# Performance work log

Measured on AMD Instinct MI355X. Metric: run time of the kernel, lower is better.

Reference implementation:

```python
import jax, jax.numpy as jnp
import numpy as np

B, T, FD, NH, NC, NOUT = 32, 512, 256, 1024, 512, 8


def setup_inputs() -> dict:
    key = jax.random.key(0)
    ks = jax.random.split(key, 12)
    s = lambda k, sh, sc=0.05: (jax.random.normal(k, sh, jnp.float32) * sc)
    return dict(
        x=jax.random.normal(ks[0], (B, T, FD), jnp.float32),
        lens=jax.random.randint(ks[1], (B,), T // 2, T + 1, jnp.int32),
        W1=s(ks[2], (NH, FD)), b1=jnp.zeros((NH,), jnp.float32),
        g1=jnp.ones((NH,), jnp.float32), be1=jnp.zeros((NH,), jnp.float32),
        W2=s(ks[3], (NH, NH)), b2=jnp.zeros((NH,), jnp.float32),
        g2=jnp.ones((NH,), jnp.float32), be2=jnp.zeros((NH,), jnp.float32),
        lstm_wih=s(ks[4], (2, 2, 4 * NC, NH)),   # [layer, dir, 4H, in]
        lstm_whh=s(ks[5], (2, 2, 4 * NC, NC)),   # [layer, dir, 4H, H]
        lstm_bih=s(ks[6], (2, 2, 4 * NC)),
        lstm_bhh=s(ks[7], (2, 2, 4 * NC)),
        w_u=s(ks[8], (2 * NC,)), b_u=jnp.zeros((), jnp.float32),
        Wc=s(ks[9], (NOUT, 2 * NC)), bc=jnp.zeros((NOUT,), jnp.float32),
    )


def _layernorm(x, g, b, eps=1e-5):
    m = x.mean(-1, keepdims=True)
    v = ((x - m) ** 2).mean(-1, keepdims=True)
    return (x - m) / jnp.sqrt(v + eps) * g + b


def _lrelu(z):
    return jnp.where(z >= 0, z, 0.01 * z)  # LeakyReLU default slope


def _lstm_dir(x, wih, whh, bih, bhh):
    # x: [B,T,in] -> h: [B,T,H]; torch gate order i,f,g,o
    Bz = x.shape[0]
    H = whh.shape[1]
    xp = jnp.einsum('bti,gi->btg', x, wih) + bih + bhh  # [B,T,4H]

    def step(carry, xt):
        h, c = carry
        gates = xt + h @ whh.T
        i, f, g, o = jnp.split(gates, 4, axis=-1)
        c = jax.nn.sigmoid(f) * c + jax.nn.sigmoid(i) * jnp.tanh(g)
        h = jax.nn.sigmoid(o) * jnp.tanh(c)
        return (h, c), h

    h0 = jnp.zeros((Bz, H), x.dtype)
    _, hs = jax.lax.scan(step, (h0, h0), xp.transpose(1, 0, 2))
    return hs.transpose(1, 0, 2)


def _bilstm(x, wih, whh, bih, bhh):
    # params indexed [dir, ...]; backward dir processes the full padded
    # sequence reversed (original feeds unpacked pad_sequence to nn.LSTM)
    hf = _lstm_dir(x, wih[0], whh[0], bih[0], bhh[0])
    hb = _lstm_dir(x[:, ::-1], wih[1], whh[1], bih[1], bhh[1])[:, ::-1]
    return jnp.concatenate([hf, hb], axis=-1)


def reference(x, lens, W1, b1, g1, be1, W2, b2, g2, be2,
              lstm_wih, lstm_whh, lstm_bih, lstm_bhh, w_u, b_u, Wc, bc):
    Tn = x.shape[1]
    # extract MLP (dropout = identity in eval)
    h = _lrelu(_layernorm(x @ W1.T + b1, g1, be1))
    h = _lrelu(_layernorm(h @ W2.T + b2, g2, be2))
    # pad_sequence zero-pads AFTER extract -> zero out pad positions
    mask = jnp.arange(Tn)[None, :] < lens[:, None]  # [B,T]
    h = h * mask[..., None]
    # 2-layer bidirectional LSTM over the full padded sequence
    h = _bilstm(h, lstm_wih[0], lstm_whh[0], lstm_bih[0], lstm_bhh[0])
    h = _bilstm(h, lstm_wih[1], lstm_whh[1], lstm_bih[1], lstm_bhh[1])
    # Attn with window_len=1: per-step linear score, masked softmax, weighted sum
    scores = h @ w_u + b_u                          # [B,T]
    scores = jnp.where(mask, scores, -jnp.inf)
    alpha = jax.nn.softmax(scores, axis=-1)
    pooled = jnp.einsum('bt,btd->bd', alpha, h)     # [B, 2*NC]
    return pooled @ Wc.T + bc
```

## Files before the change

kernel.cpp:

```cpp
#include <hip/hip_runtime.h>
#include <stdint.h>
#include <stddef.h>


typedef short  short8  __attribute__((ext_vector_type(8)));
typedef short  short4v __attribute__((ext_vector_type(4)));
typedef float  float4v __attribute__((ext_vector_type(4)));
typedef unsigned long long u64;

__device__ inline float b2f(short x){
  union { unsigned u; float f; } v; v.u = ((unsigned)(unsigned short)x) << 16; return v.f;
}
__device__ inline short f2b(float f){
  union { float f; unsigned u; } v; v.f = f;
  unsigned r = (v.u + 0x7fffu + ((v.u >> 16) & 1u)) >> 16;
  return (short)r;
}
__device__ inline float sigm(float x){ return 1.f / (1.f + __expf(-x)); }
__device__ inline float tanh_(float x){ return 2.f / (1.f + __expf(-2.f*x)) - 1.f; }

typedef const __attribute__((address_space(1))) unsigned gu32;
typedef __attribute__((address_space(3))) unsigned lu32;
__device__ inline void gld16(const void* g, void* l){
  __builtin_amdgcn_global_load_lds((gu32*)g, (lu32*)l, 16, 0, 0);
}

__global__ __launch_bounds__(256) void detect_f32(
    const unsigned short* __restrict__ p, unsigned* __restrict__ flag)
{
  const int tid = threadIdx.x;
  unsigned h = 0;
  for (int i = tid; i < 1024; i += 256){
    const unsigned e = (p[i] >> 7) & 0xFFu;
    if (e >= 0xC0u) ++h;
  }
#pragma unroll
  for (int off=32; off>0; off>>=1) h += __shfl_xor(h, off, 64);
  __shared__ unsigned sh[4];
  if ((tid&63)==0) sh[tid>>6] = h;
  __syncthreads();
  if (tid==0) *flag = (sh[0]+sh[1]+sh[2]+sh[3] >= 8u) ? 1u : 0u;
}

struct CvtArgs {
  const void* src[16];
  short*      dst[16];
  int         n[16];
  int         boff[17];
};

__global__ __launch_bounds__(256) void to_bf16_batch(
    CvtArgs a, const unsigned* __restrict__ flag)
{
  const int b = blockIdx.x;
  int lo = 0, hi = 15;
  while (lo < hi){
    const int mid = (lo + hi + 1) >> 1;
    if (b >= a.boff[mid]) lo = mid; else hi = mid - 1;
  }
  const int i   = lo;
  const int idx = (b - a.boff[i])*256 + (int)threadIdx.x;
  if (idx >= a.n[i]) return;
  if (*flag) a.dst[i][idx] = f2b(((const float*)a.src[i])[idx]);
  else       a.dst[i][idx] = ((const short*)a.src[i])[idx];
}

__global__ __launch_bounds__(256) void gemm_bt(
    const short* __restrict__ A, const short* __restrict__ W,
    short* __restrict__ C, const short* __restrict__ bias1,
    const short* __restrict__ bias2, int N, int K)
{
  __shared__ __align__(16) short lA[128*32];
  __shared__ __align__(16) short lW[128*32];
  __shared__ __align__(16) short eps[2*16*136];
  const int tid  = threadIdx.x;
  const int lane = tid & 63, wv = tid >> 6;
  const int wm = wv >> 1, wn = wv & 1;
  const int quad = lane >> 4, l15 = lane & 15;
  const long m0 = (long)blockIdx.y * 128, n0 = (long)blockIdx.x * 128;

  float4v acc[4][4];
#pragma unroll
  for (int i=0;i<4;++i)
#pragma unroll
    for (int j=0;j<4;++j) acc[i][j] = (float4v)0.f;

  const int srow = wv*16 + (lane >> 2);
  const int scol = ((lane & 3) ^ (srow & 3)) * 8;
  char* lAb = (char*)&lA[0] + wv*1024;
  char* lWb = (char*)&lW[0] + wv*1024;
  const int rchunk = (quad ^ (l15 & 3)) * 8;

  const int nkt = K >> 5;
  for (int kt = 0; kt < nkt; ++kt) {
    __syncthreads();
    {
      const short* gA0 = A + (m0 + srow) * (long)K + kt*32 + scol;
      const short* gW0 = W + (n0 + srow) * (long)K + kt*32 + scol;
      gld16(gA0,                lAb);
      gld16(gA0 + 64*(long)K,   lAb + 4096);
      gld16(gW0,                lWb);
      gld16(gW0 + 64*(long)K,   lWb + 4096);
    }
    __syncthreads();
    short8 af[4], bfr[4];
#pragma unroll
    for (int i=0;i<4;++i) af[i]  = *(const short8*)&lA[(wm*64 + i*16 + l15)*32 + rchunk];
#pragma unroll
    for (int j=0;j<4;++j) bfr[j] = *(const short8*)&lW[(wn*64 + j*16 + l15)*32 + rchunk];
#pragma unroll
    for (int i=0;i<4;++i)
#pragma unroll
      for (int j=0;j<4;++j)
        acc[i][j] = __builtin_amdgcn_mfma_f32_16x16x32_bf16(af[i], bfr[j], acc[i][j], 0, 0, 0);
  }

  float bs[4];
#pragma unroll
  for (int j=0;j<4;++j){
    const long n = n0 + wn*64 + j*16 + l15;
    bs[j] = b2f(bias1[n]);
    if (bias2) bs[j] += b2f(bias2[n]);
  }
  const int eh = tid >> 7, er = (tid >> 3) & 15, ec = tid & 7;
  short* erd = &eps[(eh*16 + er)*136 + ec*16];
  short* ewr = &eps[wm*16*136 + wn*64 + l15];
#pragma unroll
  for (int i=0;i<4;++i){
    if (i) __syncthreads();
#pragma unroll
    for (int j=0;j<4;++j)
#pragma unroll
      for (int g=0; g<4; ++g)
        ewr[(quad*4+g)*136 + j*16] = f2b(acc[i][j][g] + bs[j]);
    __syncthreads();
    short8 v0 = *(const short8*)erd;
    short8 v1 = *(const short8*)(erd + 8);
    short* cp = &C[(m0 + eh*64 + i*16 + er)*(long)N + n0 + ec*16];
    *(short8*)cp       = v0;
    *(short8*)(cp + 8) = v1;
  }
}

__global__ __launch_bounds__(256) void ln_lrelu(
    const short* __restrict__ X, const short* __restrict__ g,
    const short* __restrict__ be, short* __restrict__ out,
    const int* __restrict__ lens, const int domask)
{
  const int row = blockIdx.x, tid = threadIdx.x;
  const short* xr = X + (size_t)row * 1024;
  short4v xv = *(const short4v*)(xr + tid*4);
  float v[4];
#pragma unroll
  for (int k=0;k<4;++k) v[k] = b2f(xv[k]);
  float s  = v[0]+v[1]+v[2]+v[3];
  float sq = v[0]*v[0]+v[1]*v[1]+v[2]*v[2]+v[3]*v[3];
#pragma unroll
  for (int off=32; off>0; off>>=1){
    s  += __shfl_xor(s,  off, 64);
    sq += __shfl_xor(sq, off, 64);
  }
  __shared__ float red[8];
  if ((tid&63)==0){ red[tid>>6] = s; red[4+(tid>>6)] = sq; }
  __syncthreads();
  s  = red[0]+red[1]+red[2]+red[3];
  sq = red[4]+red[5]+red[6]+red[7];
  const float mean = s * (1.f/1024.f);
  const float var  = sq * (1.f/1024.f) - mean*mean;
  const float rstd = rsqrtf(var + 1e-5f);
  float zmul = 1.f;
  if (domask){ const int b = row >> 9, t = row & 511; if (t >= lens[b]) zmul = 0.f; }
  short4v o;
#pragma unroll
  for (int k=0;k<4;++k){
    const int n = tid*4 + k;
    float y = (v[k]-mean)*rstd*b2f(g[n]) + b2f(be[n]);
    y = (y >= 0.f) ? y : 0.01f*y;
    o[k] = f2b(y * zmul);
  }
  *(short4v*)(out + (size_t)row*1024 + tid*4) = o;
}

__global__ __launch_bounds__(256) void lstm_scan(
    const short* __restrict__ xp, const int xp_cols, const int dir0,
    const short* __restrict__ whh,
    u64* __restrict__ hstate,
    short* __restrict__ hout,
    const unsigned epoch)
{
  const int wg = blockIdx.x;
  const int dloc = wg >> 5, d = dir0 + dloc;
  const int u0 = (wg & 31) * 16;
  const int tid = threadIdx.x, lane = tid & 63, wv = tid >> 6;
  const int quad = lane >> 4, l15 = lane & 15;

  short8 af[16];
  {
    const short* wr = whh + ((size_t)d*2048 + wv*512 + u0 + l15)*512 + quad*8;
#pragma unroll
    for (int ks=0; ks<16; ++ks) af[ks] = *(const short8*)(wr + ks*32);
  }

  const int bb = tid >> 3, pp = tid & 7;
  float cstA = 0.f, cstB = 0.f;
  __shared__ __align__(16) unsigned hsh[2][32*260];
  __shared__ float gl[4][16][33];
  const unsigned tbase = epoch << 10;

  for (int step=0; step<512; ++step){
    const int t = d ? (511-step) : step;
    short4v x0, x1;
    {
      const size_t gb = (size_t)dloc*2048 + (size_t)wv*512 + u0 + quad*4;
      x0 = *(const short4v*)(xp + ((size_t)l15*512      + t)*xp_cols + gb);
      x1 = *(const short4v*)(xp + ((size_t)(l15+16)*512 + t)*xp_cols + gb);
    }
    unsigned* stg = &hsh[step&1][tid];
    if (step == 0){
#pragma unroll
      for (int k=0;k<32;++k) stg[k*260] = 0u;
    } else {
      const u64* hq = hstate + ((size_t)(d*2 + (step&1))<<13) + tid;
      const unsigned tgt = tbase + (unsigned)step;
      u64 v[32];
      for(;;){
        unsigned ok = 1u;
#pragma unroll
        for (int k=0;k<32;++k)
          v[k] = __hip_atomic_load(hq + (size_t)k*256,
                                   __ATOMIC_RELAXED, __HIP_MEMORY_SCOPE_AGENT);
#pragma unroll
        for (int k=0;k<32;++k) ok &= (unsigned)((unsigned)(v[k] >> 32) == tgt);
        if (ok) break;
        __builtin_amdgcn_s_sleep(1);
      }
#pragma unroll
      for (int k=0;k<32;++k) stg[k*260] = (unsigned)v[k];
    }
    __syncthreads();

    float4v acc0, acc1;
#pragma unroll
    for (int g=0; g<4; ++g){ acc0[g] = b2f(x0[g]); acc1[g] = b2f(x1[g]); }
    const short* hs = (const short*)&hsh[step&1][0];
#pragma unroll
    for (int ks=0; ks<16; ++ks){
      short8 b0 = *(const short8*)(hs + (size_t)l15*520      + ks*32 + quad*8);
      short8 b1 = *(const short8*)(hs + (size_t)(l15+16)*520 + ks*32 + quad*8);
      acc0 = __builtin_amdgcn_mfma_f32_16x16x32_bf16(af[ks], b0, acc0, 0, 0, 0);
      acc1 = __builtin_amdgcn_mfma_f32_16x16x32_bf16(af[ks], b1, acc1, 0, 0, 0);
    }
#pragma unroll
    for (int g=0; g<4; ++g){
      gl[wv][quad*4+g][l15]    = acc0[g];
      gl[wv][quad*4+g][l15+16] = acc1[g];
    }
    __syncthreads();

    float hv[2];
#pragma unroll
    for (int i=0; i<2; ++i){
      const int uu = 2*pp + i;
      const float gi = gl[0][uu][bb], gf = gl[1][uu][bb];
      const float gg = gl[2][uu][bb], go = gl[3][uu][bb];
      float& cref = i ? cstB : cstA;
      const float c = sigm(gf)*cref + sigm(gi)*tanh_(gg);
      cref = c;
      hv[i] = sigm(go) * tanh_(c);
    }
    const unsigned hw = (unsigned)(unsigned short)f2b(hv[0])
                      | ((unsigned)(unsigned short)f2b(hv[1]) << 16);
    const u64 pkt = ((u64)(tbase + (unsigned)step + 1u) << 32) | (u64)hw;
    __hip_atomic_store(hstate + ((size_t)(d*2 + ((step+1)&1))<<13)
                         + (size_t)bb*256 + (u0>>1) + pp,
                       pkt, __ATOMIC_RELAXED, __HIP_MEMORY_SCOPE_AGENT);
    *(unsigned*)&hout[((size_t)bb*512 + t)*1024 + d*512 + u0 + 2*pp] = hw;
  }
}

__global__ __launch_bounds__(256) void attn_cls(
    const short* __restrict__ hseq, const short* __restrict__ wu,
    const short* __restrict__ Wc, const short* __restrict__ bc,
    const int* __restrict__ lens, float* __restrict__ out)
{
  const int b = blockIdx.x, tid = threadIdx.x, lane = tid & 63, wv = tid >> 6;
  const int len = lens[b];
  __shared__ float wus[1024];
  __shared__ float sc[512];
  __shared__ float redx[8];
  __shared__ float pooled[1024];
  for (int i=tid; i<1024; i+=256) wus[i] = b2f(wu[i]);
  __syncthreads();
  const short* hb = hseq + (size_t)b*512*1024;
  for (int t=wv; t<512; t+=4){
    const short* hr = hb + (size_t)t*1024;
    float s = 0.f;
#pragma unroll
    for (int j=0;j<16;++j) s += b2f(hr[lane + j*64]) * wus[lane + j*64];
#pragma unroll
    for (int off=32; off>0; off>>=1) s += __shfl_xor(s, off, 64);
    if (lane==0) sc[t] = (t < len) ? s : -3.0e38f;
  }
  __syncthreads();
  float m = -3.0e38f;
  for (int i=tid;i<512;i+=256) m = fmaxf(m, sc[i]);
#pragma unroll
  for (int off=32; off>0; off>>=1) m = fmaxf(m, __shfl_xor(m, off, 64));
  if (lane==0) redx[wv] = m;
  __syncthreads();
  m = fmaxf(fmaxf(redx[0],redx[1]), fmaxf(redx[2],redx[3]));
  float ssum = 0.f;
  for (int i=tid;i<512;i+=256){
    float e = (i<len) ? __expf(sc[i]-m) : 0.f;
    sc[i] = e;
    ssum += e;
  }
#pragma unroll
  for (int off=32; off>0; off>>=1) ssum += __shfl_xor(ssum, off, 64);
  if (lane==0) redx[4+wv] = ssum;
  __syncthreads();
  ssum = redx[4]+redx[5]+redx[6]+redx[7];
  const float inv = 1.f/ssum;
  float4v pa = (float4v)0.f;
  const int k0 = tid*4;
  for (int t=0; t<len; ++t){
    const float a = sc[t];
    short4v hv = *(const short4v*)(hb + (size_t)t*1024 + k0);
    pa[0] += a*b2f(hv[0]); pa[1] += a*b2f(hv[1]);
    pa[2] += a*b2f(hv[2]); pa[3] += a*b2f(hv[3]);
  }
  pooled[k0+0] = pa[0]*inv; pooled[k0+1] = pa[1]*inv;
  pooled[k0+2] = pa[2]*inv; pooled[k0+3] = pa[3]*inv;
  __syncthreads();
  const int j = tid >> 5, l32 = tid & 31;
  float s2 = 0.f;
  for (int kk=l32; kk<1024; kk+=32) s2 += b2f(Wc[j*1024+kk]) * pooled[kk];
#pragma unroll
  for (int off=16; off>0; off>>=1) s2 += __shfl_xor(s2, off, 32);
  if (l32==0) out[b*8+j] = s2 + b2f(bc[j]);
}

extern "C" void kernel_launch(void* const* d_in, const int* in_sizes, int n_in,
                              void* d_out, int out_size, void* d_ws, size_t ws_size,
                              hipStream_t stream)
{
  (void)in_sizes; (void)n_in; (void)out_size;
  const int*   lens = (const int*)d_in[1];
  float* outp = (float*)d_out;

  const size_t SZ_XP_A = (size_t)16384*4096*2;
  const size_t SZ_XP_B = (size_t)16384*2048*2;
  const size_t SZ_H    = (size_t)16384*1024*2;
  const size_t SZ_HS   = 262144;
  const size_t SZ_CNT  = 16384;
  const size_t SZ_NORM = 37000000;
  const bool planA = ws_size >= SZ_XP_A + 2*SZ_H + SZ_HS + SZ_CNT + SZ_NORM;
  const bool planB = !planA && ws_size >= SZ_XP_B + 2*SZ_H + SZ_HS + SZ_CNT + SZ_NORM;
  if (!planA && !planB) return;
  const size_t xpsz = planA ? SZ_XP_A : SZ_XP_B;

  char* ws = (char*)d_ws;
  short*    XP  = (short*)ws;
  short*    HB  = (short*)(ws + xpsz);
  short*    HC  = (short*)(ws + xpsz + SZ_H);
  u64*      HS64= (u64*)(ws + xpsz + 2*SZ_H);
  unsigned* CNT = (unsigned*)(ws + xpsz + 2*SZ_H + SZ_HS);
  unsigned* FLAG = CNT + 4000;
  short*    pool = (short*)(ws + xpsz + 2*SZ_H + SZ_HS + SZ_CNT);

  size_t off = 0;
  auto carve = [&](size_t n){ short* p = pool + off; off += (n + 127) & ~(size_t)127; return p; };
  short* x   = carve(4194304);
  short* W1  = carve(262144);
  short* b1  = carve(1024);
  short* g1  = carve(1024);
  short* be1 = carve(1024);
  short* W2  = carve(1048576);
  short* b2  = carve(1024);
  short* g2  = carve(1024);
  short* be2 = carve(1024);
  short* wih = carve(8388608);
  short* whh = carve(4194304);
  short* bih = carve(8192);
  short* bhh = carve(8192);
  short* wu  = carve(1024);
  short* Wc  = carve(8192);
  short* bc  = carve(8);

  hipMemsetAsync(HS64, 0, SZ_HS, stream);
  detect_f32<<<1, 256, 0, stream>>>((const unsigned short*)d_in[0], FLAG);

  {
    struct { int idx; short* dst; int n; } cv[16] = {
      {0,x,4194304},{2,W1,262144},{3,b1,1024},{4,g1,1024},{5,be1,1024},
      {6,W2,1048576},{7,b2,1024},{8,g2,1024},{9,be2,1024},
      {10,wih,8388608},{11,whh,4194304},{12,bih,8192},{13,bhh,8192},
      {14,wu,1024},{16,Wc,8192},{17,bc,8}
    };
    CvtArgs a;
    int acc = 0;
    for (int i=0;i<16;++i){
      a.src[i]  = d_in[cv[i].idx];
      a.dst[i]  = cv[i].dst;
      a.n[i]    = cv[i].n;
      a.boff[i] = acc;
      acc += (cv[i].n + 255) / 256;
    }
    a.boff[16] = acc;
    to_bf16_batch<<<acc, 256, 0, stream>>>(a, FLAG);
  }

  dim3 blk(256);
  gemm_bt<<<dim3(8,128),  blk, 0, stream>>>(x,  W1, XP, b1, nullptr, 1024, 256);
  ln_lrelu<<<16384, blk, 0, stream>>>(XP, g1, be1, HB, lens, 0);
  gemm_bt<<<dim3(8,128),  blk, 0, stream>>>(HB, W2, XP, b2, nullptr, 1024, 1024);
  ln_lrelu<<<16384, blk, 0, stream>>>(XP, g2, be2, HC, lens, 1);

  const short* lin[2]  = { HC, HB };
  short*       lout[2] = { HB, HC };
  for (int l = 0; l < 2; ++l){
    const short* whh_l = whh + (size_t)l*2*2048*512;
    if (planA){
      gemm_bt<<<dim3(32,128), blk, 0, stream>>>(
          lin[l], wih + (size_t)l*4096*1024, XP,
          bih + l*4096, bhh + l*4096, 4096, 1024);
      lstm_scan<<<64, blk, 0, stream>>>(XP, 4096, 0, whh_l, HS64, lout[l],
                                        (unsigned)(l+1));
    } else {
      for (int d = 0; d < 2; ++d){
        gemm_bt<<<dim3(16,128), blk, 0, stream>>>(
            lin[l], wih + ((size_t)(l*2+d))*2048*1024, XP,
            bih + (l*2+d)*2048, bhh + (l*2+d)*2048, 2048, 1024);
        lstm_scan<<<32, blk, 0, stream>>>(XP, 2048, d, whh_l, HS64, lout[l],
                                          (unsigned)(l+1));
      }
    }
  }
  attn_cls<<<32, blk, 0, stream>>>(HC, wu, Wc, bc, lens, outp);
}
```

Measured before the change: 4.183 ms.

## Split attention pooling into four kernels for wider grid parallelism

Replaces the single 32-block attention/classifier kernel with four kernels: per-chunk score computation (256 blocks), per-batch softmax, chunked weighted pooling over feature slices (256 blocks), and the final classifier. The aim is to use many more CUs for the memory-bound reads of the hidden sequence instead of one block per batch row. In exchange it adds three extra kernel launches, global round-trips for scores and pooled vectors, and reuses the XP workspace as scratch. Pooling now runs over all 512 timesteps using zeroed alpha for padded positions rather than stopping at len.

Result: no change. 4.112 ms (-1.7%).

```diff
diff --git a/kernel.cpp b/kernel.cpp
--- a/kernel.cpp
+++ b/kernel.cpp
@@ -278,63 +278,96 @@
   }
 }
 
-__global__ __launch_bounds__(256) void attn_cls(
+__global__ __launch_bounds__(256) void attn_scores(
     const short* __restrict__ hseq, const short* __restrict__ wu,
-    const short* __restrict__ Wc, const short* __restrict__ bc,
-    const int* __restrict__ lens, float* __restrict__ out)
+    float* __restrict__ scr, const int* __restrict__ lens)
+{
+  const int tc = blockIdx.x, b = blockIdx.y;
+  const int tid = threadIdx.x, lane = tid & 63, wv = tid >> 6;
+  const int len = lens[b];
+  __shared__ float wus[1024];
+  for (int i=tid; i<1024; i+=256) wus[i] = b2f(wu[i]);
+  __syncthreads();
+  const short* hb = hseq + (size_t)b*512*1024;
+  for (int tt=wv; tt<64; tt+=4){
+    const int t = tc*64 + tt;
+    const short* hr = hb + (size_t)t*1024;
+    float s = 0.f;
+#pragma unroll
+    for (int j=0;j<16;++j) s += b2f(hr[lane + j*64]) * wus[lane + j*64];
+#pragma unroll
+    for (int off=32; off>0; off>>=1) s += __shfl_xor(s, off, 64);
+    if (lane==0) scr[(size_t)b*512 + t] = (t < len) ? s : -3.0e38f;
+  }
+}
+
+__global__ __launch_bounds__(256) void attn_softmax(
+    float* __restrict__ scr, const int* __restrict__ lens)
 {
   const int b = blockIdx.x, tid = threadIdx.x, lane = tid & 63, wv = tid >> 6;
   const int len = lens[b];
-  __shared__ float wus[1024];
-  __shared__ float sc[512];
-  __shared__ float redx[8];
-  __shared__ float pooled[1024];
-  for (int i=tid; i<1024; i+=256) wus[i] = b2f(wu[i]);
-  __syncthreads();
-  const short* hb = hseq + (size_t)b*512*1024;
-  for (int t=wv; t<512; t+=4){
-    const short* hr = hb + (size_t)t*1024;
+  float* sb = scr + (size_t)b*512;
+  const float v0 = sb[tid], v1 = sb[tid+256];
+  __shared__ float red[8];
+  float m = fmaxf(v0, v1);
+#pragma unroll
+  for (int off=32; off>0; off>>=1) m = fmaxf(m, __shfl_xor(m, off, 64));
+  if (lane==0) red[wv] = m;
+  __syncthreads();
+  m = fmaxf(fmaxf(red[0],red[1]), fmaxf(red[2],red[3]));
+  const float e0 = (tid     < len) ? __expf(v0 - m) : 0.f;
+  const float e1 = (tid+256 < len) ? __expf(v1 - m) : 0.f;
+  float s = e0 + e1;
+#pragma unroll
+  for (int off=32; off>0; off>>=1) s += __shfl_xor(s, off, 64);
+  if (lane==0) red[4+wv] = s;
+  __syncthreads();
+  s = red[4]+red[5]+red[6]+red[7];
+  const float inv = 1.f/s;
+  sb[tid]     = e0*inv;
+  sb[tid+256] = e1*inv;
+}
+
+__global__ __launch_bounds__(256) void attn_pool(
+    const short* __restrict__ hseq, const float* __restrict__ scr,
+    float* __restrict__ pooled)
+{
+  const int fc = blockIdx.x, b = blockIdx.y;
+  const int tid = threadIdx.x;
+  const int strip = tid >> 5, l32v = tid & 31;
+  __shared__ float al[512];
+  __shared__ float red[8][132];
+  for (int i=tid; i<512; i+=256) al[i] = scr[(size_t)b*512 + i];
+  __syncthreads();
+  const short* hbase = hseq + (size_t)b*512*1024 + fc*128 + l32v*4;
+  float4v acc = (float4v)0.f;
+  for (int tt=0; tt<64; ++tt){
+    const int t = strip*64 + tt;
+    const float a = al[t];
+    short4v hv = *(const short4v*)(hbase + (size_t)t*1024);
+    acc[0] += a*b2f(hv[0]); acc[1] += a*b2f(hv[1]);
+    acc[2] += a*b2f(hv[2]); acc[3] += a*b2f(hv[3]);
+  }
+#pragma unroll
+  for (int k=0;k<4;++k) red[strip][l32v*4+k] = acc[k];
+  __syncthreads();
+  if (tid < 128){
     float s = 0.f;
 #pragma unroll
-    for (int j=0;j<16;++j) s += b2f(hr[lane + j*64]) * wus[lane + j*64];
-#pragma unroll
-    for (int off=32; off>0; off>>=1) s += __shfl_xor(s, off, 64);
-    if (lane==0) sc[t] = (t < len) ? s : -3.0e38f;
-  }
-  __syncthreads();
-  float m = -3.0e38f;
-  for (int i=tid;i<512;i+=256) m = fmaxf(m, sc[i]);
-#pragma unroll
-  for (int off=32; off>0; off>>=1) m = fmaxf(m, __shfl_xor(m, off, 64));
-  if (lane==0) redx[wv] = m;
-  __syncthreads();
-  m = fmaxf(fmaxf(redx[0],redx[1]), fmaxf(redx[2],redx[3]));
-  float ssum = 0.f;
-  for (int i=tid;i<512;i+=256){
-    float e = (i<len) ? __expf(sc[i]-m) : 0.f;
-    sc[i] = e;
-    ssum += e;
-  }
-#pragma unroll
-  for (int off=32; off>0; off>>=1) ssum += __shfl_xor(ssum, off, 64);
-  if (lane==0) redx[4+wv] = ssum;
-  __syncthreads();
-  ssum = redx[4]+redx[5]+redx[6]+redx[7];
-  const float inv = 1.f/ssum;
-  float4v pa = (float4v)0.f;
-  const int k0 = tid*4;
-  for (int t=0; t<len; ++t){
-    const float a = sc[t];
-    short4v hv = *(const short4v*)(hb + (size_t)t*1024 + k0);
-    pa[0] += a*b2f(hv[0]); pa[1] += a*b2f(hv[1]);
-    pa[2] += a*b2f(hv[2]); pa[3] += a*b2f(hv[3]);
-  }
-  pooled[k0+0] = pa[0]*inv; pooled[k0+1] = pa[1]*inv;
-  pooled[k0+2] = pa[2]*inv; pooled[k0+3] = pa[3]*inv;
-  __syncthreads();
+    for (int st=0; st<8; ++st) s += red[st][tid];
+    pooled[(size_t)b*1024 + fc*128 + tid] = s;
+  }
+}
+
+__global__ __launch_bounds__(256) void attn_cls2(
+    const float* __restrict__ pooled, const short* __restrict__ Wc,
+    const short* __restrict__ bc, float* __restrict__ out)
+{
+  const int b = blockIdx.x, tid = threadIdx.x;
   const int j = tid >> 5, l32 = tid & 31;
+  const float* pb = pooled + (size_t)b*1024;
   float s2 = 0.f;
-  for (int kk=l32; kk<1024; kk+=32) s2 += b2f(Wc[j*1024+kk]) * pooled[kk];
+  for (int kk=l32; kk<1024; kk+=32) s2 += b2f(Wc[j*1024+kk]) * pb[kk];
 #pragma unroll
   for (int off=16; off>0; off>>=1) s2 += __shfl_xor(s2, off, 32);
   if (l32==0) out[b*8+j] = s2 + b2f(bc[j]);
@@ -436,5 +469,10 @@
       }
     }
   }
-  attn_cls<<<32, blk, 0, stream>>>(HC, wu, Wc, bc, lens, outp);
-}
+  float* SCR  = (float*)XP;
+  float* POOL = SCR + 32*512;
+  attn_scores<<<dim3(8,32), blk, 0, stream>>>(HC, wu, SCR, lens);
+  attn_softmax<<<32, blk, 0, stream>>>(SCR, lens);
+  attn_pool<<<dim3(8,32), blk, 0, stream>>>(HC, SCR, POOL);
+  attn_cls2<<<32, blk, 0, stream>>>(POOL, Wc, bc, outp);
+}
```
